# Performance work log

Measured on AMD Instinct MI355X. Metric: run time of the kernel, lower is better.

## Reference

```python
import jax, jax.numpy as jnp
import numpy as np

B, C, H, W = 8, 128, 64, 64


def setup_inputs() -> dict:
    key = jax.random.key(0)
    ks = jax.random.split(key, 4)
    s = 1.0 / np.sqrt(C)
    return {
        "x": jax.random.normal(ks[0], (B, C, H, W), dtype=jnp.float32),
        "Wq": jax.random.normal(ks[1], (C, C), dtype=jnp.float32) * s,
        "bq": jnp.zeros((C,), dtype=jnp.float32),
        "Wk": jax.random.normal(ks[2], (C, C), dtype=jnp.float32) * s,
        "bk": jnp.zeros((C,), dtype=jnp.float32),
        "Wv": jax.random.normal(ks[3], (C, C), dtype=jnp.float32) * s,
        "bv": jnp.zeros((C,), dtype=jnp.float32),
    }


def reference(x, Wq, bq, Wk, bk, Wv, bv):
    b, c, h, w = x.shape
    xf = x.reshape(b, c, h * w)  # [B, C, N]
    # 1x1 convs are per-pixel CxC matmuls (weight[out,in] contracted over in)
    q = jnp.einsum("oc,bcn->bon", Wq, xf) + bq[None, :, None]
    k = jnp.einsum("oc,bcn->bon", Wk, xf) + bk[None, :, None]
    v = jnp.einsum("oc,bcn->bon", Wv, xf) + bv[None, :, None]
    scale = 1.0 / jnp.sqrt(jnp.asarray(c, dtype=x.dtype))
    attn = jnp.einsum("bcn,bcm->bnm", q, k) * scale  # [B, N, N]
    attn = jax.nn.softmax(attn, axis=-1)
    out = jnp.einsum("bnm,bcm->bcn", attn, v)  # [B, C, N]
    return out.reshape(b, c, h, w) + x
```

## Files before the change

### kernel.cpp

```cpp
#include <hip/hip_runtime.h>

#define B_ 8
#define C_ 128
#define N_ 4096
#define SCALE 0.08838834764831845f

typedef __attribute__((ext_vector_type(8))) short short8;
typedef __attribute__((ext_vector_type(4))) short short4v;
typedef __attribute__((ext_vector_type(4))) float f32x4;

__device__ inline float b2f(unsigned short u) {
    union { unsigned int i; float f; } v; v.i = ((unsigned int)u) << 16; return v.f;
}
__device__ inline unsigned short f2b(float f) {
    unsigned int x = __float_as_uint(f);
    return (unsigned short)((x + 0x7FFFu + ((x >> 16) & 1u)) >> 16);
}

__device__ inline void gld_lds16(const void* g, void* l) {
    __builtin_amdgcn_global_load_lds(
        (const __attribute__((address_space(1))) unsigned int*)g,
        (__attribute__((address_space(3))) unsigned int*)l, 16, 0, 0);
}

__global__ __launch_bounds__(256) void qkv_mfma(
    const float* __restrict__ x,
    const float* __restrict__ Wq, const float* __restrict__ bq,
    const float* __restrict__ Wk, const float* __restrict__ bk,
    const float* __restrict__ Wv, const float* __restrict__ bv,
    float* __restrict__ q, unsigned short* __restrict__ kTs,
    unsigned short* __restrict__ vS)
{
    __shared__ __align__(16) short Xs[64 * 128];
    __shared__ __align__(16) float Obuf[64 * 132];

    const int t    = threadIdx.x;
    const int w    = t >> 6;
    const int lane = t & 63;
    const int l15  = lane & 15;
    const int quad = lane >> 4;

    const int b  = blockIdx.x & 7;
    const int n0 = (blockIdx.x >> 3) * 64;
    const long base = (long)b * C_ * N_;

    auto load_af = [&](const float* __restrict__ W, short8 (&af)[2][4]) {
        #pragma unroll
        for (int ot = 0; ot < 2; ++ot) {
            const int o = 32 * w + 16 * ot + l15;
            #pragma unroll
            for (int ks = 0; ks < 4; ++ks) {
                const float4 a0 = *(const float4*)(const void*)(W + o * C_ + ks * 32 + quad * 8);
                const float4 a1 = *(const float4*)(const void*)(W + o * C_ + ks * 32 + quad * 8 + 4);
                short8 f;
                f[0] = (short)f2b(a0.x); f[1] = (short)f2b(a0.y);
                f[2] = (short)f2b(a0.z); f[3] = (short)f2b(a0.w);
                f[4] = (short)f2b(a1.x); f[5] = (short)f2b(a1.y);
                f[6] = (short)f2b(a1.z); f[7] = (short)f2b(a1.w);
                af[ot][ks] = f;
            }
        }
    };

    auto mfma_pass = [&](const short8 (&af)[2][4], f32x4 (&acc)[2][4]) {
        #pragma unroll
        for (int ot = 0; ot < 2; ++ot)
            #pragma unroll
            for (int nt = 0; nt < 4; ++nt)
                acc[ot][nt] = (f32x4){0.f, 0.f, 0.f, 0.f};
        #pragma unroll
        for (int nt = 0; nt < 4; ++nt) {
            const int n = nt * 16 + l15;
            short8 bx[4];
            #pragma unroll
            for (int ks = 0; ks < 4; ++ks)
                bx[ks] = *(const short8*)(const void*)(Xs + n * 128 + (((ks * 4 + quad) ^ l15) << 3));
            #pragma unroll
            for (int ot = 0; ot < 2; ++ot)
                #pragma unroll
                for (int ks = 0; ks < 4; ++ks)
                    acc[ot][nt] = __builtin_amdgcn_mfma_f32_16x16x32_bf16(af[ot][ks], bx[ks], acc[ot][nt], 0, 0, 0);
        }
    };

    short8 afA[2][4], afB[2][4];
    load_af(Wq, afA);

    #pragma unroll
    for (int it = 0; it < 8; ++it) {
        const int c  = (t >> 4) + it * 16;
        const int n4 = (t & 15) * 4;
        const float4 xv = *(const float4*)(const void*)(x + base + (long)c * N_ + n0 + n4);
        const int bc = c >> 3, cl = c & 7;
        Xs[(n4 + 0) * 128 + ((bc ^ ((n4 + 0) & 15)) << 3) + cl] = (short)f2b(xv.x);
        Xs[(n4 + 1) * 128 + ((bc ^ ((n4 + 1) & 15)) << 3) + cl] = (short)f2b(xv.y);
        Xs[(n4 + 2) * 128 + ((bc ^ ((n4 + 2) & 15)) << 3) + cl] = (short)f2b(xv.z);
        Xs[(n4 + 3) * 128 + ((bc ^ ((n4 + 3) & 15)) << 3) + cl] = (short)f2b(xv.w);
    }
    __syncthreads();

    {
        load_af(Wv, afB);
        f32x4 acc[2][4];
        mfma_pass(afA, acc);
        #pragma unroll
        for (int ot = 0; ot < 2; ++ot)
            #pragma unroll
            for (int r = 0; r < 4; ++r) {
                const int o = 32 * w + 16 * ot + quad * 4 + r;
                const float bb = bq[o];
                #pragma unroll
                for (int nt = 0; nt < 4; ++nt)
                    q[base + (long)o * N_ + n0 + nt * 16 + l15] = (acc[ot][nt][r] + bb) * SCALE;
            }
    }

    {
        load_af(Wk, afA);
        f32x4 acc[2][4];
        mfma_pass(afB, acc);
        #pragma unroll
        for (int ot = 0; ot < 2; ++ot)
            #pragma unroll
            for (int r = 0; r < 4; ++r) {
                const int o = 32 * w + 16 * ot + quad * 4 + r;
                const float bb = bv[o];
                const int sw = ((o >> 1) & 3) << 3;
                #pragma unroll
                for (int nt = 0; nt < 4; ++nt) {
                    const int n = nt * 16 + l15;
                    const int ns = (n & 32) | ((((n >> 3) & 3) << 3) ^ sw) | (n & 7);
                    vS[base + (long)o * N_ + n0 + ns] = f2b(acc[ot][nt][r] + bb);
                }
            }
    }

    {
        f32x4 acc[2][4];
        mfma_pass(afA, acc);
        #pragma unroll
        for (int ot = 0; ot < 2; ++ot)
            #pragma unroll
            for (int r = 0; r < 4; ++r) {
                const int o = 32 * w + 16 * ot + quad * 4 + r;
                const float bb = bk[o];
                #pragma unroll
                for (int nt = 0; nt < 4; ++nt) {
                    const int n = nt * 16 + l15;
                    Obuf[n * 132 + (((o >> 3) ^ l15) << 3) + (o & 7)] = acc[ot][nt][r] + bb;
                }
            }
        __syncthreads();
        const int n = t >> 2, oh = (t & 3) * 32;
        #pragma unroll
        for (int i = 0; i < 32; i += 4) {
            const float4 kv = *(const float4*)(const void*)(Obuf + n * 132 + oh + i);
            short4v s;
            s[0] = (short)f2b(kv.x); s[1] = (short)f2b(kv.y);
            s[2] = (short)f2b(kv.z); s[3] = (short)f2b(kv.w);
            *(short4v*)(void*)(kTs + base + (long)(n0 + n) * C_ + oh + i) = s;
        }
    }
}

__global__ __launch_bounds__(512) void attn_mfma(
    const float* qg,
    const unsigned short* __restrict__ kTs,
    const unsigned short* __restrict__ vS,
    const float* __restrict__ xg,
    float* out)
{
    __shared__ union {
        struct {
            short K[2][2][4096];
            short V[2][2][4096];
            short Pb[8][16 * 40];
        } s;
        float Ot[64 * 130];
    } sm;
    __shared__ float Ls[2][4][16];
    __shared__ float linvA[64];

    const int t    = threadIdx.x;
    const int w    = t >> 6;
    const int g    = w >> 2;
    const int wq   = w & 3;
    const int lane = t & 63;
    const int l15  = lane & 15;
    const int quad = lane >> 4;

    const int b  = blockIdx.x & 7;
    const int n0 = (blockIdx.x >> 3) * 64;
    const long base = (long)b * C_ * N_;

    const int query = n0 + 16 * wq + l15;
    short8 qf[4];
    #pragma unroll
    for (int ks = 0; ks < 4; ++ks) {
        short8 f;
        #pragma unroll
        for (int j = 0; j < 8; ++j) {
            const int c = ks * 32 + quad * 8 + j;
            f[j] = (short)f2b(qg[base + (long)c * N_ + query]);
        }
        qf[ks] = f;
    }

    f32x4 acc[8];
    #pragma unroll
    for (int ct = 0; ct < 8; ++ct) acc[ct] = (f32x4){0.f, 0.f, 0.f, 0.f};
    f32x4 accS = (f32x4){0.f, 0.f, 0.f, 0.f};
    short8 ones;
    #pragma unroll
    for (int j = 0; j < 8; ++j) ones[j] = (short)0x3F80;

    auto stage = [&](int buf, int pair) {
        const int mt = pair * 2 + g;
        const char* gK = (const char*)(kTs + base + (long)mt * 32 * C_);
        char* lK = (char*)sm.s.K[buf][g];
        char* lV = (char*)sm.s.V[buf][g];
        #pragma unroll
        for (int jj = 0; jj < 2; ++jj) {
            const int d = wq * 2048 + jj * 1024;
            gld_lds16(gK + d + lane * 16, lK + d);
            const int dv = d + lane * 16;
            const int c  = dv >> 6;
            gld_lds16((const char*)(vS + base + (long)c * N_ + mt * 32) + (dv & 63), lV + d);
        }
    };

    auto compute = [&](int buf) {
        const short* Kb = sm.s.K[buf][g];
        const short* Vb = sm.s.V[buf][g];
        f32x4 sc[2];
        sc[0] = (f32x4){0.f, 0.f, 0.f, 0.f};
        sc[1] = (f32x4){0.f, 0.f, 0.f, 0.f};
        #pragma unroll
        for (int kt = 0; kt < 2; ++kt) {
            const int row = (kt * 16 + l15) * 128;
            #pragma unroll
            for (int ks = 0; ks < 4; ++ks) {
                const short8 kf = *(const short8*)(const void*)(Kb + row + (((ks * 4 + quad) ^ l15) << 3));
                sc[kt] = __builtin_amdgcn_mfma_f32_16x16x32_bf16(qf[ks], kf, sc[kt], 0, 0, 0);
            }
        }
        short* Pw = sm.s.Pb[w];
        #pragma unroll
        for (int kt = 0; kt < 2; ++kt)
            #pragma unroll
            for (int r = 0; r < 4; ++r)
                Pw[(quad * 4 + r) * 40 + kt * 16 + l15] = (short)f2b(__expf(sc[kt][r]));
        const short8 pf = *(const short8*)(const void*)(Pw + l15 * 40 + quad * 8);
        accS = __builtin_amdgcn_mfma_f32_16x16x32_bf16(pf, ones, accS, 0, 0, 0);
        #pragma unroll
        for (int ct = 0; ct < 8; ++ct) {
            const short8 vf = *(const short8*)(const void*)(Vb + (ct * 16 + l15) * 32 + ((quad ^ ((l15 >> 1) & 3)) << 3));
            acc[ct] = __builtin_amdgcn_mfma_f32_16x16x32_bf16(pf, vf, acc[ct], 0, 0, 0);
        }
    };

    stage(0, 0);
    __syncthreads();
    for (int i = 0; i < 64; ++i) {
        if (i < 63) stage((i + 1) & 1, i + 1);
        compute(i & 1);
        __syncthreads();
    }

    if (l15 == 0) {
        #pragma unroll
        for (int r = 0; r < 4; ++r) Ls[g][wq][quad * 4 + r] = accS[r];
    }
    if (g == 0) {
        #pragma unroll
        for (int ct = 0; ct < 8; ++ct)
            #pragma unroll
            for (int r = 0; r < 4; ++r)
                sm.Ot[(16 * wq + quad * 4 + r) * 130 + ct * 16 + l15] = acc[ct][r];
    }
    __syncthreads();
    if (g == 1) {
        #pragma unroll
        for (int ct = 0; ct < 8; ++ct)
            #pragma unroll
            for (int r = 0; r < 4; ++r)
                sm.Ot[(16 * wq + quad * 4 + r) * 130 + ct * 16 + l15] += acc[ct][r];
    } else if (l15 == 0) {
        #pragma unroll
        for (int r = 0; r < 4; ++r) {
            const int row = 16 * wq + quad * 4 + r;
            linvA[row] = 1.0f / fmaxf(Ls[0][wq][quad * 4 + r] + Ls[1][wq][quad * 4 + r], 1e-20f);
        }
    }
    __syncthreads();

    const int c  = t >> 2;
    const int nh = (t & 3) * 16;
    const long gb = base + (long)c * N_ + n0 + nh;
    #pragma unroll
    for (int i = 0; i < 16; i += 4) {
        const float4 xs = *(const float4*)(const void*)(xg + gb + i);
        float4 rv;
        rv.x = sm.Ot[(nh + i + 0) * 130 + c] * linvA[nh + i + 0] + xs.x;
        rv.y = sm.Ot[(nh + i + 1) * 130 + c] * linvA[nh + i + 1] + xs.y;
        rv.z = sm.Ot[(nh + i + 2) * 130 + c] * linvA[nh + i + 2] + xs.z;
        rv.w = sm.Ot[(nh + i + 3) * 130 + c] * linvA[nh + i + 3] + xs.w;
        *(float4*)(void*)(out + gb + i) = rv;
    }
}

extern "C" void kernel_launch(void* const* d_in, const int* in_sizes, int n_in,
                              void* d_out, int out_size, void* d_ws, size_t ws_size,
                              hipStream_t stream) {
    const float* x  = (const float*)d_in[0];
    const float* Wq = (const float*)d_in[1];
    const float* bq = (const float*)d_in[2];
    const float* Wk = (const float*)d_in[3];
    const float* bk = (const float*)d_in[4];
    const float* Wv = (const float*)d_in[5];
    const float* bv = (const float*)d_in[6];
    float* out = (float*)d_out;

    const long BCN = (long)B_ * C_ * N_;
    unsigned short* kTs = (unsigned short*)d_ws;
    unsigned short* vS  = kTs + BCN;

    qkv_mfma<<<512, 256, 0, stream>>>(x, Wq, bq, Wk, bk, Wv, bv, out, kTs, vS);
    attn_mfma<<<B_ * (N_ / 64), 512, 0, stream>>>(out, kTs, vS, x, out);
}
```

Baseline: 195.1 us.

## Split QKV projection across blocks per weight and tighten attention pipeline waits

The QKV kernel now launches three times as many blocks, and each block computes only one of Q, V or K. This is meant to raise parallelism and cut register pressure. K is written straight from registers into a swizzled transposed layout, so the LDS staging buffer and its extra barrier are gone. In the attention loop, __syncthreads is replaced by explicit vmcnt waits plus raw s_barrier, and the MFMA sections get s_setprio to favour matrix issue. The trade-offs are that each block reloads and converts its x tile (redundant x reads), and the K stores change to a swizzled layout that the attention kernel's reads must match.

```diff
diff --git a/kernel.cpp b/kernel.cpp
--- a/kernel.cpp
+++ b/kernel.cpp
@@ -32,7 +32,6 @@
     unsigned short* __restrict__ vS)
 {
     __shared__ __align__(16) short Xs[64 * 128];
-    __shared__ __align__(16) float Obuf[64 * 132];
 
     const int t    = threadIdx.x;
     const int w    = t >> 6;
@@ -40,51 +39,33 @@
     const int l15  = lane & 15;
     const int quad = lane >> 4;
 
-    const int b  = blockIdx.x & 7;
-    const int n0 = (blockIdx.x >> 3) * 64;
+    const int b    = blockIdx.x & 7;
+    const int rest = blockIdx.x >> 3;
+    const int p    = rest >> 6;
+    const int n0   = (rest & 63) * 64;
     const long base = (long)b * C_ * N_;
 
-    auto load_af = [&](const float* __restrict__ W, short8 (&af)[2][4]) {
-        #pragma unroll
-        for (int ot = 0; ot < 2; ++ot) {
-            const int o = 32 * w + 16 * ot + l15;
-            #pragma unroll
-            for (int ks = 0; ks < 4; ++ks) {
-                const float4 a0 = *(const float4*)(const void*)(W + o * C_ + ks * 32 + quad * 8);
-                const float4 a1 = *(const float4*)(const void*)(W + o * C_ + ks * 32 + quad * 8 + 4);
-                short8 f;
-                f[0] = (short)f2b(a0.x); f[1] = (short)f2b(a0.y);
-                f[2] = (short)f2b(a0.z); f[3] = (short)f2b(a0.w);
-                f[4] = (short)f2b(a1.x); f[5] = (short)f2b(a1.y);
-                f[6] = (short)f2b(a1.z); f[7] = (short)f2b(a1.w);
-                af[ot][ks] = f;
-            }
-        }
-    };
-
-    auto mfma_pass = [&](const short8 (&af)[2][4], f32x4 (&acc)[2][4]) {
-        #pragma unroll
-        for (int ot = 0; ot < 2; ++ot)
-            #pragma unroll
-            for (int nt = 0; nt < 4; ++nt)
-                acc[ot][nt] = (f32x4){0.f, 0.f, 0.f, 0.f};
-        #pragma unroll
-        for (int nt = 0; nt < 4; ++nt) {
-            const int n = nt * 16 + l15;
-            short8 bx[4];
-            #pragma unroll
-            for (int ks = 0; ks < 4; ++ks)
-                bx[ks] = *(const short8*)(const void*)(Xs + n * 128 + (((ks * 4 + quad) ^ l15) << 3));
-            #pragma unroll
-            for (int ot = 0; ot < 2; ++ot)
-                #pragma unroll
-                for (int ks = 0; ks < 4; ++ks)
-                    acc[ot][nt] = __builtin_amdgcn_mfma_f32_16x16x32_bf16(af[ot][ks], bx[ks], acc[ot][nt], 0, 0, 0);
-        }
-    };
-
-    short8 afA[2][4], afB[2][4];
-    load_af(Wq, afA);
+    const float* W; const float* bias;
+    if (p == 0)      { W = Wq; bias = bq; }
+    else if (p == 1) { W = Wv; bias = bv; }
+    else             { W = Wk; bias = bk; }
+
+    short8 af[2][4];
+    #pragma unroll
+    for (int ot = 0; ot < 2; ++ot) {
+        const int o = 32 * w + 16 * ot + l15;
+        #pragma unroll
+        for (int ks = 0; ks < 4; ++ks) {
+            const float4 a0 = *(const float4*)(const void*)(W + o * C_ + ks * 32 + quad * 8);
+            const float4 a1 = *(const float4*)(const void*)(W + o * C_ + ks * 32 + quad * 8 + 4);
+            short8 f;
+            f[0] = (short)f2b(a0.x); f[1] = (short)f2b(a0.y);
+            f[2] = (short)f2b(a0.z); f[3] = (short)f2b(a0.w);
+            f[4] = (short)f2b(a1.x); f[5] = (short)f2b(a1.y);
+            f[6] = (short)f2b(a1.z); f[7] = (short)f2b(a1.w);
+            af[ot][ks] = f;
+        }
+    }
 
     #pragma unroll
     for (int it = 0; it < 8; ++it) {
@@ -99,66 +80,73 @@
     }
     __syncthreads();
 
-    {
-        load_af(Wv, afB);
-        f32x4 acc[2][4];
-        mfma_pass(afA, acc);
+    f32x4 acc[2][4];
+    #pragma unroll
+    for (int ot = 0; ot < 2; ++ot)
+        #pragma unroll
+        for (int nt = 0; nt < 4; ++nt)
+            acc[ot][nt] = (f32x4){0.f, 0.f, 0.f, 0.f};
+    #pragma unroll
+    for (int nt = 0; nt < 4; ++nt) {
+        const int n = nt * 16 + l15;
+        short8 bx[4];
+        #pragma unroll
+        for (int ks = 0; ks < 4; ++ks)
+            bx[ks] = *(const short8*)(const void*)(Xs + n * 128 + (((ks * 4 + quad) ^ l15) << 3));
         #pragma unroll
         for (int ot = 0; ot < 2; ++ot)
             #pragma unroll
+            for (int ks = 0; ks < 4; ++ks)
+                acc[ot][nt] = __builtin_amdgcn_mfma_f32_16x16x32_bf16(af[ot][ks], bx[ks], acc[ot][nt], 0, 0, 0);
+    }
+
+    if (p == 0) {
+        #pragma unroll
+        for (int ot = 0; ot < 2; ++ot) {
+            const int O0 = 32 * w + 16 * ot + quad * 4;
+            const float4 bb = *(const float4*)(const void*)(bias + O0);
+            #pragma unroll
             for (int r = 0; r < 4; ++r) {
-                const int o = 32 * w + 16 * ot + quad * 4 + r;
-                const float bb = bq[o];
+                const float br = r == 0 ? bb.x : r == 1 ? bb.y : r == 2 ? bb.z : bb.w;
                 #pragma unroll
                 for (int nt = 0; nt < 4; ++nt)
-                    q[base + (long)o * N_ + n0 + nt * 16 + l15] = (acc[ot][nt][r] + bb) * SCALE;
+                    q[base + (long)(O0 + r) * N_ + n0 + nt * 16 + l15] = (acc[ot][nt][r] + br) * SCALE;
             }
-    }
-
-    {
-        load_af(Wk, afA);
-        f32x4 acc[2][4];
-        mfma_pass(afB, acc);
-        #pragma unroll
-        for (int ot = 0; ot < 2; ++ot)
+        }
+    } else if (p == 1) {
+        #pragma unroll
+        for (int ot = 0; ot < 2; ++ot) {
+            const int O0 = 32 * w + 16 * ot + quad * 4;
+            const float4 bb = *(const float4*)(const void*)(bias + O0);
             #pragma unroll
             for (int r = 0; r < 4; ++r) {
-                const int o = 32 * w + 16 * ot + quad * 4 + r;
-                const float bb = bv[o];
+                const float br = r == 0 ? bb.x : r == 1 ? bb.y : r == 2 ? bb.z : bb.w;
+                const int o  = O0 + r;
                 const int sw = ((o >> 1) & 3) << 3;
                 #pragma unroll
                 for (int nt = 0; nt < 4; ++nt) {
                     const int n = nt * 16 + l15;
                     const int ns = (n & 32) | ((((n >> 3) & 3) << 3) ^ sw) | (n & 7);
-                    vS[base + (long)o * N_ + n0 + ns] = f2b(acc[ot][nt][r] + bb);
+                    vS[base + (long)o * N_ + n0 + ns] = f2b(acc[ot][nt][r] + br);
                 }
             }
-    }
-
-    {
-        f32x4 acc[2][4];
-        mfma_pass(afA, acc);
-        #pragma unroll
-        for (int ot = 0; ot < 2; ++ot)
-            #pragma unroll
-            for (int r = 0; r < 4; ++r) {
-                const int o = 32 * w + 16 * ot + quad * 4 + r;
-                const float bb = bk[o];
-                #pragma unroll
-                for (int nt = 0; nt < 4; ++nt) {
-                    const int n = nt * 16 + l15;
-                    Obuf[n * 132 + (((o >> 3) ^ l15) << 3) + (o & 7)] = acc[ot][nt][r] + bb;
-                }
+        }
+    } else {
+        #pragma unroll
+        for (int ot = 0; ot < 2; ++ot) {
+            const int O0 = 32 * w + 16 * ot + quad * 4;
+            const float4 bb = *(const float4*)(const void*)(bias + O0);
+            #pragma unroll
+            for (int nt = 0; nt < 4; ++nt) {
+                const int n = nt * 16 + l15;
+                short4v s;
+                s[0] = (short)f2b(acc[ot][nt][0] + bb.x);
+                s[1] = (short)f2b(acc[ot][nt][1] + bb.y);
+                s[2] = (short)f2b(acc[ot][nt][2] + bb.z);
+                s[3] = (short)f2b(acc[ot][nt][3] + bb.w);
+                *(short4v*)(void*)(kTs + base + (long)(n0 + n) * C_
+                                   + (((O0 >> 3) ^ l15) << 3) + (O0 & 7)) = s;
             }
-        __syncthreads();
-        const int n = t >> 2, oh = (t & 3) * 32;
-        #pragma unroll
-        for (int i = 0; i < 32; i += 4) {
-            const float4 kv = *(const float4*)(const void*)(Obuf + n * 132 + oh + i);
-            short4v s;
-            s[0] = (short)f2b(kv.x); s[1] = (short)f2b(kv.y);
-            s[2] = (short)f2b(kv.z); s[3] = (short)f2b(kv.w);
-            *(short4v*)(void*)(kTs + base + (long)(n0 + n) * C_ + oh + i) = s;
         }
     }
 }
@@ -235,6 +223,7 @@
         f32x4 sc[2];
         sc[0] = (f32x4){0.f, 0.f, 0.f, 0.f};
         sc[1] = (f32x4){0.f, 0.f, 0.f, 0.f};
+        __builtin_amdgcn_s_setprio(1);
         #pragma unroll
         for (int kt = 0; kt < 2; ++kt) {
             const int row = (kt * 16 + l15) * 128;
@@ -244,6 +233,7 @@
                 sc[kt] = __builtin_amdgcn_mfma_f32_16x16x32_bf16(qf[ks], kf, sc[kt], 0, 0, 0);
             }
         }
+        __builtin_amdgcn_s_setprio(0);
         short* Pw = sm.s.Pb[w];
         #pragma unroll
         for (int kt = 0; kt < 2; ++kt)
@@ -251,20 +241,27 @@
             for (int r = 0; r < 4; ++r)
                 Pw[(quad * 4 + r) * 40 + kt * 16 + l15] = (short)f2b(__expf(sc[kt][r]));
         const short8 pf = *(const short8*)(const void*)(Pw + l15 * 40 + quad * 8);
+        __builtin_amdgcn_s_setprio(1);
         accS = __builtin_amdgcn_mfma_f32_16x16x32_bf16(pf, ones, accS, 0, 0, 0);
         #pragma unroll
         for (int ct = 0; ct < 8; ++ct) {
             const short8 vf = *(const short8*)(const void*)(Vb + (ct * 16 + l15) * 32 + ((quad ^ ((l15 >> 1) & 3)) << 3));
             acc[ct] = __builtin_amdgcn_mfma_f32_16x16x32_bf16(pf, vf, acc[ct], 0, 0, 0);
         }
+        __builtin_amdgcn_s_setprio(0);
     };
 
     stage(0, 0);
-    __syncthreads();
     for (int i = 0; i < 64; ++i) {
-        if (i < 63) stage((i + 1) & 1, i + 1);
+        if (i < 63) {
+            stage((i + 1) & 1, i + 1);
+            asm volatile("s_waitcnt vmcnt(4)" ::: "memory");
+        } else {
+            asm volatile("s_waitcnt vmcnt(0)" ::: "memory");
+        }
+        __builtin_amdgcn_s_barrier();
         compute(i & 1);
-        __syncthreads();
+        __builtin_amdgcn_s_barrier();
     }
 
     if (l15 == 0) {
@@ -325,6 +322,6 @@
     unsigned short* kTs = (unsigned short*)d_ws;
     unsigned short* vS  = kTs + BCN;
 
-    qkv_mfma<<<512, 256, 0, stream>>>(x, Wq, bq, Wk, bk, Wv, bv, out, kTs, vS);
+    qkv_mfma<<<1536, 256, 0, stream>>>(x, Wq, bq, Wk, bk, Wv, bv, out, kTs, vS);
     attn_mfma<<<B_ * (N_ / 64), 512, 0, stream>>>(out, kTs, vS, x, out);
 }
```

New measurement: 199.8 us. 2.4% more time.
